# Kernel optimization log

Hardware: AMD Instinct MI355X
Metric: run time of the kernel (lower is better)

The kernel has to match this reference:

```python
import jax, jax.numpy as jnp
import numpy as np

B, T, BIN, D, S, L = 128, 512, 24, 256, 128, 2
MAX_LEN = 512.0   # config.max_length, used as attention score scale
EPS = 1e-6
P = 3.0           # GeM pooling power


def _sinusoid(t, dim, min_ts=1.0, max_ts=10000.0):
    # half sin / half cos geometric timescales (min_timescale..max_timescale)
    num = dim // 2
    inv = min_ts * jnp.exp(jnp.arange(num, dtype=jnp.float32) * (-np.log(max_ts / min_ts) / max(num - 1, 1)))
    ang = jnp.arange(t, dtype=jnp.float32)[:, None] * inv[None, :]        # [T, dim/2]
    return jnp.concatenate([jnp.sin(ang), jnp.cos(ang)], axis=-1)          # [T, dim]


def _rope(x):
    # rotate-half RoPE over last dim, positions along axis -2
    t, d = x.shape[-2], x.shape[-1]
    inv = 1.0 / (10000.0 ** (jnp.arange(0, d, 2, dtype=jnp.float32) / d))  # [d/2]
    ang = jnp.arange(t, dtype=jnp.float32)[:, None] * inv[None, :]         # [T, d/2]
    sin = jnp.concatenate([jnp.sin(ang), jnp.sin(ang)], axis=-1)
    cos = jnp.concatenate([jnp.cos(ang), jnp.cos(ang)], axis=-1)
    x1, x2 = jnp.split(x, 2, axis=-1)
    return x * cos + jnp.concatenate([-x2, x1], axis=-1) * sin


def setup_inputs() -> dict:
    key = jax.random.key(0)
    ks = jax.random.split(key, 12)
    std_in = 1.0 / np.sqrt(BIN)
    std_d = 1.0 / np.sqrt(D)
    return {
        "x": jax.random.uniform(ks[0], (B, T, BIN), dtype=jnp.float32),
        "pe_scale": jnp.ones((), jnp.float32),                                  # learnable PE scale
        "W_in": jax.random.normal(ks[1], (BIN, D), jnp.float32) * std_in,        # encoder_start
        "b_in": jnp.zeros((D,), jnp.float32),
        "norm_scale": jnp.ones((L,), jnp.float32),                               # ScaledNorm scalar per layer
        "W1": jax.random.normal(ks[2], (L, D, 2 * D + S), jnp.float32) * std_d,  # GAU in-proj
        "b1": jnp.zeros((L, 2 * D + S), jnp.float32),
        "gamma": jnp.ones((L, 2, S), jnp.float32),                               # q/k offset-scale
        "beta": jnp.zeros((L, 2, S), jnp.float32),
        "W2": jax.random.normal(ks[3], (L, D, D), jnp.float32) * std_d,          # GAU out-proj
        "b2": jnp.zeros((L, D), jnp.float32),
        "We": jax.random.normal(ks[4], (D, D), jnp.float32) * std_d,             # metric embedding
        "be": jnp.zeros((D,), jnp.float32),
    }


def reference(x, pe_scale, W_in, b_in, norm_scale, W1, b1, gamma, beta, W2, b2, We, be):
    # scaled sinusoidal positional embedding (additive)
    h = x + pe_scale * _sinusoid(x.shape[1], x.shape[2])
    # encoder start + swish
    h = jax.nn.swish(h @ W_in + b_in)                                   # [B,T,D]
    for i in range(L):  # GAU stack (attention-free gated attention units)
        shortcut = h
        hn = h * jax.lax.rsqrt(jnp.mean(h * h, axis=-1, keepdims=True) + EPS) * norm_scale[i]
        uv = jax.nn.swish(hn @ W1[i] + b1[i])                           # [B,T,2D+S]
        u, v, base = uv[..., :D], uv[..., D:2 * D], uv[..., 2 * D:]
        q = _rope(base * gamma[i, 0] + beta[i, 0])                      # [B,T,S]
        k = _rope(base * gamma[i, 1] + beta[i, 1])
        scores = jnp.einsum('bnd,bmd->bnm', q, k) / MAX_LEN             # [B,T,T]
        attn = jnp.square(jax.nn.relu(scores))                          # SqrReLU
        out = u * jnp.einsum('bnm,bme->bne', attn, v)                   # gated attention output
        h = shortcut + out @ W2[i] + b2[i]
    unpooled = h
    # generalized-mean pooling over sequence (p=3, clamp for stability)
    pooled = jnp.mean(jnp.clip(h, EPS, None) ** P, axis=1) ** (1.0 / P)  # [B,D]
    # metric embedding: linear + L2 normalize
    emb = pooled @ We + be
    emb = emb / jnp.linalg.norm(emb, axis=-1, keepdims=True)
    return emb, unpooled
```

## Files before the change

kernel.cpp:

```cpp
#include <hip/hip_runtime.h>
#include <hip/hip_bf16.h>

#define B_ 128
#define T_ 512
#define BIN_ 24
#define D_ 256
#define S_ 128
#define L_ 2
#define BT_ (B_*T_)

typedef __hip_bfloat16 bf16;
typedef __hip_bfloat162 bf162;
typedef __attribute__((ext_vector_type(8))) short bf16x8;
typedef __attribute__((ext_vector_type(4))) short s16x4;
typedef __attribute__((ext_vector_type(4))) float f32x4;

__device__ __forceinline__ float b2f(bf16 x){ return __bfloat162float(x); }
__device__ __forceinline__ bf16 f2b(float x){ return __float2bfloat16(x); }
__device__ __forceinline__ float swish(float v){
  float e = __builtin_amdgcn_exp2f(-1.442695040888963f * v);
  return v * __builtin_amdgcn_rcpf(1.f + e);
}
__device__ __forceinline__ void gld16(const bf16* g, bf16* l){
  __builtin_amdgcn_global_load_lds(
      (const __attribute__((address_space(1))) void*)g,
      (__attribute__((address_space(3))) void*)l, 16, 0, 0);
}

__global__ void tables_kernel(const float* pe_scale_ptr, float* pe_tab, float* rs, float* rc) {
  int t = blockIdx.x;
  int j = threadIdx.x;
  float ps = pe_scale_ptr[0];
  const float LOG1E4 = 9.210340371976184f;
  if (j < 64) {
    float inv = expf(-LOG1E4 * (float)j / 64.f);
    float ang = (float)t * inv;
    rs[t*64 + j] = sinf(ang);
    rc[t*64 + j] = cosf(ang);
  }
  if (j < BIN_) {
    int jj = (j < 12) ? j : (j - 12);
    float inv = expf(-LOG1E4 * (float)jj / 11.f);
    float ang = (float)t * inv;
    pe_tab[t*BIN_ + j] = ps * ((j < 12) ? sinf(ang) : cosf(ang));
  }
}

__global__ __launch_bounds__(256) void prep_kernel(const float* W1, const float* W2,
                                                   bf16* W1t, bf16* W2t) {
  int idx = blockIdx.x*256 + threadIdx.x;
  if (idx < 2*256*640) {
    int l = idx / (256*640); int rem = idx % (256*640);
    int k = rem / 640; int n = rem % 640;
    W1t[(size_t)l*640*256 + n*256 + k] = f2b(W1[idx]);
  }
  if (idx < 2*256*256) {
    int l = idx >> 16; int rem = idx & 65535;
    int k = rem >> 8; int n = rem & 255;
    W2t[(size_t)l*65536 + n*256 + k] = f2b(W2[idx]);
  }
}

__global__ __launch_bounds__(256) void init_kernel(float* rms1, float* pooled_raw) {
  int i = blockIdx.x*256 + threadIdx.x;
  if (i < BT_) rms1[i] = 0.f;
  if (i < B_*D_) pooled_raw[i] = 0.f;
}

__global__ __launch_bounds__(256) void embed_kernel(const float* x, const float* pe_tab,
                const float* W_in, const float* b_in, float* rms0, bf16* hb) {
  __shared__ float xr[8][BIN_];
  __shared__ float wsum[4][8];
  int tid = threadIdx.x;
  int row0 = blockIdx.x * 8;
  if (tid < 8*BIN_) {
    int r = tid / BIN_, k = tid % BIN_;
    int row = row0 + r;
    int t = row & (T_-1);
    xr[r][k] = x[(size_t)row*BIN_ + k] + pe_tab[t*BIN_ + k];
  }
  __syncthreads();
  int d = tid;
  float bi = b_in[d];
  float acc[8];
  #pragma unroll
  for (int r=0;r<8;r++) acc[r]=bi;
  #pragma unroll
  for (int k=0;k<BIN_;k++){
    float w = W_in[k*D_ + d];
    #pragma unroll
    for (int r=0;r<8;r++) acc[r] += xr[r][k]*w;
  }
  float sq[8];
  #pragma unroll
  for (int r=0;r<8;r++){
    float v = swish(acc[r]);
    hb[(size_t)(row0+r)*D_ + d] = f2b(v);
    sq[r] = v*v;
  }
  #pragma unroll
  for (int off=1; off<64; off<<=1)
    #pragma unroll
    for (int r=0;r<8;r++) sq[r] += __shfl_xor(sq[r], off);
  if ((tid&63)==0)
    #pragma unroll
    for (int r=0;r<8;r++) wsum[tid>>6][r] = sq[r];
  __syncthreads();
  if (tid < 8) rms0[row0+tid] = wsum[0][tid]+wsum[1][tid]+wsum[2][tid]+wsum[3][tid];
}

__global__ __launch_bounds__(256) void gemm1_mfma(const bf16* A, const bf16* Bt,
      const float* bias, const float* rmsraw, const float* norm_scale, int l,
      bf16* u, bf16* Vtg, bf16* basebuf) {
  __shared__ char smem[34816];
  bf16* As  = (bf16*)smem;
  bf16* Bs  = (bf16*)(smem + 16384);
  bf16* Ovl = (bf16*)smem;

  int tid = threadIdx.x;
  int w = tid>>6, lane = tid&63, r = lane&15, g = lane>>4;
  int wr = w>>1, wc = w&1;
  int dd = blockIdx.x; int xcd = dd&7, slot = dd>>3;
  int panel = xcd*64 + slot/5; int bx = slot%5;
  int row0 = panel*128, col0 = bx*128;

  int trl = 8*w + (lane>>3);
  int tcg = ((lane&7) ^ ((lane>>3)&7)) * 8;

  f32x4 acc[4][4];
  #pragma unroll
  for (int i=0;i<4;i++)
    #pragma unroll
    for (int j=0;j<4;j++) acc[i][j] = (f32x4){0.f,0.f,0.f,0.f};

  for (int k0=0; k0<D_; k0+=64) {
    #pragma unroll
    for (int i=0;i<4;i++){
      int tr = 32*i + trl;
      gld16(A  + (size_t)(row0+tr)*D_ + k0 + tcg, As + (32*i + 8*w)*64);
      gld16(Bt + (size_t)(col0+tr)*D_ + k0 + tcg, Bs + (32*i + 8*w)*64);
    }
    __syncthreads();
    #pragma unroll
    for (int kk=0; kk<2; kk++){
      bf16x8 a[4], b[4];
      #pragma unroll
      for (int i=0;i<4;i++){
        int ch = ((kk*4 + g) ^ (r&7)) * 8;
        a[i] = *(const bf16x8*)(As + (64*wr+16*i+r)*64 + ch);
        b[i] = *(const bf16x8*)(Bs + (64*wc+16*i+r)*64 + ch);
      }
      #pragma unroll
      for (int i=0;i<4;i++)
        #pragma unroll
        for (int j=0;j<4;j++)
          acc[i][j] = __builtin_amdgcn_mfma_f32_16x16x32_bf16(a[i], b[j], acc[i][j], 0,0,0);
    }
    __syncthreads();
  }

  float ns = norm_scale[l];
  #pragma unroll
  for (int i=0;i<4;i++){
    size_t grow0 = row0 + 64*wr + 16*i + 4*g;
    float4 rv = *(const float4*)(rmsraw + grow0);
    float sc[4];
    sc[0] = rsqrtf(rv.x*(1.f/D_) + 1e-6f) * ns;
    sc[1] = rsqrtf(rv.y*(1.f/D_) + 1e-6f) * ns;
    sc[2] = rsqrtf(rv.z*(1.f/D_) + 1e-6f) * ns;
    sc[3] = rsqrtf(rv.w*(1.f/D_) + 1e-6f) * ns;
    #pragma unroll
    for (int j=0;j<4;j++){
      int gcol = col0 + 64*wc + 16*j + r;
      float bv = bias[gcol];
      if (bx == 2 || bx == 3) {
        #pragma unroll
        for (int reg=0; reg<4; reg++){
          float v = swish(acc[i][j][reg]*sc[reg] + bv);
          Ovl[(64*wc+16*j+r)*136 + (64*wr+16*i+4*g+reg)] = f2b(v);
        }
      } else {
        #pragma unroll
        for (int reg=0; reg<4; reg++){
          float v = swish(acc[i][j][reg]*sc[reg] + bv);
          Ovl[(64*wr+16*i+4*g+reg)*136 + (64*wc+16*j+r)] = f2b(v);
        }
      }
    }
  }

  __syncthreads();
  if (bx == 2 || bx == 3) {
    size_t bb = row0 >> 9;
    int mg = row0 & 511;
    #pragma unroll
    for (int c=0;c<8;c++){
      int chunk = c*256 + tid;
      int e = chunk >> 4, mloc = (chunk & 15)*8;
      *(bf16x8*)(Vtg + bb*131072 + (size_t)(col0-256+e)*T_ + mg + mloc) =
        *(const bf16x8*)(Ovl + e*136 + mloc);
    }
  } else {
    #pragma unroll
    for (int c=0;c<8;c++){
      int chunk = c*256 + tid;
      int lr = chunk >> 4, lc = (chunk & 15)*8;
      bf16x8 v = *(const bf16x8*)(Ovl + lr*136 + lc);
      if (bx < 2)
        *(bf16x8*)(u + (size_t)(row0+lr)*D_ + col0 + lc) = v;
      else
        *(bf16x8*)(basebuf + (size_t)(row0+lr)*S_ + lc) = v;
    }
  }
}

__global__ __launch_bounds__(256) void qk_kernel(const bf16* basebuf, const float* gamma, const float* beta,
      int l, const float* rs, const float* rc, bf16* q, bf16* k) {
  int tid = threadIdx.x;
  int j = tid & 127;
  size_t row = (size_t)blockIdx.x*2 + (tid>>7);
  int t = (int)(row & (T_-1));
  int j2 = j ^ 64;
  float v0 = b2f(basebuf[row*S_ + j]);
  float v1 = b2f(basebuf[row*S_ + j2]);
  int jm = j & 63;
  float sn = rs[t*64 + jm], cs = rc[t*64 + jm];
  float sgn = (j < 64) ? -1.f : 1.f;
  const float* g  = gamma + l*2*S_;
  const float* bt = beta  + l*2*S_;
  float xq = v0*g[j]      + bt[j];
  float pq = v1*g[j2]     + bt[j2];
  q[row*S_ + j] = f2b(xq*cs + sgn*pq*sn);
  float xk = v0*g[S_+j]   + bt[S_+j];
  float pk = v1*g[S_+j2]  + bt[S_+j2];
  k[row*S_ + j] = f2b(xk*cs + sgn*pk*sn);
}

__global__ __launch_bounds__(512, 4) void attn_gemm2_fused(const bf16* q, const bf16* k,
      const bf16* Vtg, const bf16* u, const bf16* W2t, const float* bias,
      int mode, float* rms1, float* pooled_raw, float* outb, bf16* hb) {
  __shared__ char smem[67584];
  bf16* Ks = (bf16*)smem;
  bf16* Vt = (bf16*)(smem + 16384);
  bf16* Ps = (bf16*)(smem + 49152);
  bf16* Os = (bf16*)smem;

  int tid = threadIdx.x;
  int w = tid >> 6, l = tid & 63;
  int r = l & 15, g = l >> 4;
  int rgp = w & 3, eh = w >> 2;
  int xcd = blockIdx.x & 7, j0 = blockIdx.x >> 3;
  int b  = xcd*16 + (j0 >> 2);
  int nt = j0 & 3;
  size_t rowbase = (size_t)b * T_;
  int n0 = nt * 128;

  bf16x8 qf[4];
  const bf16* qrow = q + (rowbase + n0 + 16*w + r) * S_ + g*8;
  #pragma unroll
  for (int kk=0; kk<4; kk++) qf[kk] = *(const bf16x8*)(qrow + kk*32);

  f32x4 oacc[16];
  #pragma unroll
  for (int i=0;i<16;i++) oacc[i] = (f32x4){0.f,0.f,0.f,0.f};

  for (int m0 = 0; m0 < T_; m0 += 64) {
    #pragma unroll
    for (int i=0;i<2;i++){
      int chunk = i*512 + w*64 + l;
      int row = chunk >> 4, c = chunk & 15;
      gld16(k + (rowbase + m0 + row)*S_ + ((c ^ (row&7)) << 3),
            Ks + (i*512 + w*64)*8);
    }
    #pragma unroll
    for (int i=0;i<4;i++){
      int chunk = i*512 + w*64 + l;
      int e = chunk >> 3, c = chunk & 7;
      gld16(Vtg + (size_t)b*131072 + (size_t)e*T_ + m0 + ((c ^ (e&7)) << 3),
            Vt + (i*512 + w*64)*8);
    }
    __syncthreads();

    __builtin_amdgcn_s_setprio(1);
    #pragma unroll
    for (int nf=0; nf<4; nf++){
      f32x4 sacc = (f32x4){0.f,0.f,0.f,0.f};
      #pragma unroll
      for (int kk=0; kk<4; kk++){
        int ch = ((kk*4 + g) ^ (r&7)) * 8;
        bf16x8 kf = *(const bf16x8*)(Ks + (16*nf + r)*128 + ch);
        sacc = __builtin_amdgcn_mfma_f32_16x16x32_bf16(qf[kk], kf, sacc, 0,0,0);
      }
      #pragma unroll
      for (int reg=0; reg<4; reg++){
        float t = fmaxf(sacc[reg] * (1.f/512.f), 0.f);
        Ps[(16*w + 4*g + reg)*72 + 16*nf + r] = f2b(t*t);
      }
    }
    __builtin_amdgcn_s_setprio(0);
    __syncthreads();

    __builtin_amdgcn_s_setprio(1);
    #pragma unroll
    for (int ks=0; ks<2; ks++){
      bf16x8 pa0 = *(const bf16x8*)(Ps + (32*rgp      + r)*72 + ks*32 + g*8);
      bf16x8 pa1 = *(const bf16x8*)(Ps + (32*rgp + 16 + r)*72 + ks*32 + g*8);
      #pragma unroll
      for (int ef=0; ef<8; ef++){
        int e = 16*(8*eh + ef) + r;
        bf16x8 vb = *(const bf16x8*)(Vt + e*64 + (((4*ks + g) ^ (e&7)) << 3));
        oacc[ef]   = __builtin_amdgcn_mfma_f32_16x16x32_bf16(pa0, vb, oacc[ef],   0,0,0);
        oacc[8+ef] = __builtin_amdgcn_mfma_f32_16x16x32_bf16(pa1, vb, oacc[8+ef], 0,0,0);
      }
    }
    __builtin_amdgcn_s_setprio(0);
    __syncthreads();
  }

  size_t growbase = rowbase + n0;
  #pragma unroll
  for (int rr=0; rr<2; rr++)
    #pragma unroll
    for (int ef=0; ef<8; ef++)
      #pragma unroll
      for (int reg=0; reg<4; reg++)
        Os[(32*rgp + 16*rr + 4*g + reg)*264 + 16*(8*eh+ef) + r] = f2b(oacc[rr*8+ef][reg]);
  __syncthreads();
  #pragma unroll
  for (int i=0;i<8;i++){
    int chunk = i*512 + tid;
    int row = chunk >> 5, c = chunk & 31;
    bf16x8 uvv = *(const bf16x8*)(u + (growbase + row)*D_ + c*8);
    bf16x8 ov  = *(const bf16x8*)(Os + row*264 + c*8);
    bf16x8 res;
    #pragma unroll
    for (int e=0;e<8;e++)
      ((bf16*)&res)[e] = f2b(b2f(((bf16*)&ov)[e]) * b2f(((bf16*)&uvv)[e]));
    *(bf16x8*)(Os + row*264 + c*8) = res;
  }
  __syncthreads();

  f32x4 acc2[2][8];
  #pragma unroll
  for (int c2=0;c2<2;c2++)
    #pragma unroll
    for (int i=0;i<8;i++) acc2[c2][i] = (f32x4){0.f,0.f,0.f,0.f};
  __builtin_amdgcn_s_setprio(1);
  #pragma unroll
  for (int kc=0; kc<8; kc++){
    bf16x8 a0[8];
    #pragma unroll
    for (int i=0;i<8;i++)
      a0[i] = *(const bf16x8*)(Os + (16*i + r)*264 + kc*32 + g*8);
    #pragma unroll
    for (int chf=0; chf<2; chf++){
      bf16x8 wfr = *(const bf16x8*)(W2t + (size_t)(128*chf + 16*w + r)*256 + kc*32 + g*8);
      #pragma unroll
      for (int i=0;i<8;i++)
        acc2[chf][i] = __builtin_amdgcn_mfma_f32_16x16x32_bf16(a0[i], wfr, acc2[chf][i], 0,0,0);
    }
  }
  __builtin_amdgcn_s_setprio(0);

  #pragma unroll
  for (int chf=0; chf<2; chf++){
    int col = 128*chf + 16*w + r;
    float bv = bias[col];
    if (mode == 0) {
      #pragma unroll
      for (int i=0;i<8;i++){
        #pragma unroll
        for (int reg=0; reg<4; reg++){
          size_t row = growbase + 16*i + 4*g + reg;
          float hv = b2f(hb[row*D_ + col]) + acc2[chf][i][reg] + bv;
          hb[row*D_ + col] = f2b(hv);
          float ssum = hv*hv;
          ssum += __shfl_xor(ssum,1); ssum += __shfl_xor(ssum,2);
          ssum += __shfl_xor(ssum,4); ssum += __shfl_xor(ssum,8);
          if (r == 0) atomicAdd(rms1 + row, ssum);
        }
      }
    } else {
      float psum = 0.f;
      #pragma unroll
      for (int i=0;i<8;i++){
        #pragma unroll
        for (int reg=0; reg<4; reg++){
          size_t row = growbase + 16*i + 4*g + reg;
          float hv = b2f(hb[row*D_ + col]) + acc2[chf][i][reg] + bv;
          outb[row*D_ + col] = hv;
          float cv = fmaxf(hv, 1e-6f);
          psum += cv*cv*cv;
        }
      }
      psum += __shfl_xor(psum,16); psum += __shfl_xor(psum,32);
      if (g == 0) atomicAdd(pooled_raw + b*D_ + col, psum);
    }
  }
}

__global__ __launch_bounds__(256) void emb_kernel(const float* pooled_raw, const float* We,
      const float* be, float* out) {
  __shared__ float pr[D_];
  __shared__ float red[256];
  int b = blockIdx.x, j = threadIdx.x;
  pr[j] = cbrtf(pooled_raw[b*D_+j] * (1.f/T_));
  __syncthreads();
  float acc = be[j];
  for (int kk=0;kk<D_;kk++) acc += pr[kk]*We[kk*D_+j];
  red[j] = acc*acc;
  __syncthreads();
  for (int off=128; off>0; off>>=1){
    if (j<off) red[j]+=red[j+off];
    __syncthreads();
  }
  out[b*D_+j] = acc * rsqrtf(red[0]);
}

extern "C" void kernel_launch(void* const* d_in, const int* in_sizes, int n_in,
                              void* d_out, int out_size, void* d_ws, size_t ws_size,
                              hipStream_t stream) {
  const float* x         = (const float*)d_in[0];
  const float* pe_scale  = (const float*)d_in[1];
  const float* W_in      = (const float*)d_in[2];
  const float* b_in      = (const float*)d_in[3];
  const float* norm_scale= (const float*)d_in[4];
  const float* W1        = (const float*)d_in[5];
  const float* b1        = (const float*)d_in[6];
  const float* gamma     = (const float*)d_in[7];
  const float* beta      = (const float*)d_in[8];
  const float* W2        = (const float*)d_in[9];
  const float* b2        = (const float*)d_in[10];
  const float* We        = (const float*)d_in[11];
  const float* be        = (const float*)d_in[12];

  char* ws = (char*)d_ws;
  bf16*  hb      = (bf16*)(ws);
  bf16*  u       = (bf16*)(ws + 33554432);
  bf16*  Vtg     = (bf16*)(ws + 67108864);
  bf16*  basebuf = (bf16*)(ws + 100663296);
  bf16*  q       = (bf16*)(ws + 117440512);
  bf16*  kbuf    = (bf16*)(ws + 134217728);
  float* pe_tab  = (float*)(ws + 150994944);
  float* rs_tab  = (float*)(ws + 151044096);
  float* rc_tab  = (float*)(ws + 151175168);
  float* pooled_raw = (float*)(ws + 151306240);
  float* rms0    = (float*)(ws + 151437312);
  float* rms1    = (float*)(ws + 151699456);
  bf16*  W1t     = (bf16*)(ws + 151961600);
  bf16*  W2t     = (bf16*)(ws + 152616960);

  tables_kernel<<<T_, 64, 0, stream>>>(pe_scale, pe_tab, rs_tab, rc_tab);
  prep_kernel<<<1280, 256, 0, stream>>>(W1, W2, W1t, W2t);
  init_kernel<<<BT_/256, 256, 0, stream>>>(rms1, pooled_raw);
  embed_kernel<<<BT_/8, 256, 0, stream>>>(x, pe_tab, W_in, b_in, rms0, hb);
  float* outb = (float*)d_out + B_*D_;
  for (int l=0; l<L_; l++) {
    gemm1_mfma<<<BT_/128*5, 256, 0, stream>>>(hb, W1t + (size_t)l*640*D_, b1 + l*640,
        l ? rms1 : rms0, norm_scale, l, u, Vtg, basebuf);
    qk_kernel<<<BT_/2, 256, 0, stream>>>(basebuf, gamma, beta, l, rs_tab, rc_tab, q, kbuf);
    attn_gemm2_fused<<<B_*4, 512, 0, stream>>>(q, kbuf, Vtg, u,
        W2t + (size_t)l*D_*D_, b2 + l*D_, l, rms1, pooled_raw, outb, hb);
  }
  emb_kernel<<<B_, 256, 0, stream>>>(pooled_raw, We, be, (float*)d_out);
}
```

Before: 331.6 us.

## Halve attention query tile and key chunk to double block count

Reduces the fused attention+out-proj kernel's per-block query tile from 128 to 64 rows and the key/value chunk from 64 to 32, launching twice as many blocks with half the shared memory and fewer accumulators. The warp-to-work mapping, the LDS swizzles for V and the P staging stride are reworked to match. The aim is more blocks resident per CU and better latency hiding. In exchange each K/V tile is reloaded by twice as many blocks, each chunk does less MFMA work per barrier, and W2 fragments are re-read per smaller row tile.

```diff
diff --git a/kernel.cpp b/kernel.cpp
--- a/kernel.cpp
+++ b/kernel.cpp
@@ -236,81 +236,77 @@
   k[row*S_ + j] = f2b(xk*cs + sgn*pk*sn);
 }
 
-__global__ __launch_bounds__(512, 4) void attn_gemm2_fused(const bf16* q, const bf16* k,
+__global__ __launch_bounds__(512, 6) void attn_gemm2_fused(const bf16* q, const bf16* k,
       const bf16* Vtg, const bf16* u, const bf16* W2t, const float* bias,
       int mode, float* rms1, float* pooled_raw, float* outb, bf16* hb) {
-  __shared__ char smem[67584];
+  __shared__ char smem[33792];
   bf16* Ks = (bf16*)smem;
-  bf16* Vt = (bf16*)(smem + 16384);
-  bf16* Ps = (bf16*)(smem + 49152);
+  bf16* Vt = (bf16*)(smem + 8192);
+  bf16* Ps = (bf16*)(smem + 24576);
   bf16* Os = (bf16*)smem;
 
   int tid = threadIdx.x;
   int w = tid >> 6, l = tid & 63;
   int r = l & 15, g = l >> 4;
-  int rgp = w & 3, eh = w >> 2;
+  int wq = w & 3, nfh = w >> 2;
+  int rgp2 = w & 1, eh2 = w >> 1;
   int xcd = blockIdx.x & 7, j0 = blockIdx.x >> 3;
-  int b  = xcd*16 + (j0 >> 2);
-  int nt = j0 & 3;
+  int b  = xcd*16 + (j0 >> 3);
+  int nt = j0 & 7;
   size_t rowbase = (size_t)b * T_;
-  int n0 = nt * 128;
+  int n0 = nt * 64;
 
   bf16x8 qf[4];
-  const bf16* qrow = q + (rowbase + n0 + 16*w + r) * S_ + g*8;
+  const bf16* qrow = q + (rowbase + n0 + 16*wq + r) * S_ + g*8;
   #pragma unroll
   for (int kk=0; kk<4; kk++) qf[kk] = *(const bf16x8*)(qrow + kk*32);
 
-  f32x4 oacc[16];
-  #pragma unroll
-  for (int i=0;i<16;i++) oacc[i] = (f32x4){0.f,0.f,0.f,0.f};
-
-  for (int m0 = 0; m0 < T_; m0 += 64) {
+  f32x4 oacc[8];
+  #pragma unroll
+  for (int i=0;i<8;i++) oacc[i] = (f32x4){0.f,0.f,0.f,0.f};
+
+  for (int m0 = 0; m0 < T_; m0 += 32) {
+    {
+      int row = tid >> 4, c = tid & 15;
+      gld16(k + (rowbase + m0 + row)*S_ + ((c ^ (row&7)) << 3), Ks + w*512);
+    }
     #pragma unroll
     for (int i=0;i<2;i++){
-      int chunk = i*512 + w*64 + l;
-      int row = chunk >> 4, c = chunk & 15;
-      gld16(k + (rowbase + m0 + row)*S_ + ((c ^ (row&7)) << 3),
-            Ks + (i*512 + w*64)*8);
-    }
-    #pragma unroll
-    for (int i=0;i<4;i++){
-      int chunk = i*512 + w*64 + l;
-      int e = chunk >> 3, c = chunk & 7;
-      gld16(Vtg + (size_t)b*131072 + (size_t)e*T_ + m0 + ((c ^ (e&7)) << 3),
+      int chunk = i*512 + tid;
+      int e = chunk >> 2, c = chunk & 3;
+      gld16(Vtg + (size_t)b*131072 + (size_t)e*T_ + m0 + ((c ^ (e&3)) << 3),
             Vt + (i*512 + w*64)*8);
     }
     __syncthreads();
 
     __builtin_amdgcn_s_setprio(1);
-    #pragma unroll
-    for (int nf=0; nf<4; nf++){
+    {
       f32x4 sacc = (f32x4){0.f,0.f,0.f,0.f};
       #pragma unroll
       for (int kk=0; kk<4; kk++){
         int ch = ((kk*4 + g) ^ (r&7)) * 8;
-        bf16x8 kf = *(const bf16x8*)(Ks + (16*nf + r)*128 + ch);
+        bf16x8 kf = *(const bf16x8*)(Ks + (16*nfh + r)*128 + ch);
         sacc = __builtin_amdgcn_mfma_f32_16x16x32_bf16(qf[kk], kf, sacc, 0,0,0);
       }
       #pragma unroll
       for (int reg=0; reg<4; reg++){
         float t = fmaxf(sacc[reg] * (1.f/512.f), 0.f);
-        Ps[(16*w + 4*g + reg)*72 + 16*nf + r] = f2b(t*t);
+        Ps[(16*wq + 4*g + reg)*40 + 16*nfh + r] = f2b(t*t);
       }
     }
     __builtin_amdgcn_s_setprio(0);
     __syncthreads();
 
     __builtin_amdgcn_s_setprio(1);
-    #pragma unroll
-    for (int ks=0; ks<2; ks++){
-      bf16x8 pa0 = *(const bf16x8*)(Ps + (32*rgp      + r)*72 + ks*32 + g*8);
-      bf16x8 pa1 = *(const bf16x8*)(Ps + (32*rgp + 16 + r)*72 + ks*32 + g*8);
-      #pragma unroll
-      for (int ef=0; ef<8; ef++){
-        int e = 16*(8*eh + ef) + r;
-        bf16x8 vb = *(const bf16x8*)(Vt + e*64 + (((4*ks + g) ^ (e&7)) << 3));
+    {
+      bf16x8 pa0 = *(const bf16x8*)(Ps + (32*rgp2      + r)*40 + g*8);
+      bf16x8 pa1 = *(const bf16x8*)(Ps + (32*rgp2 + 16 + r)*40 + g*8);
+      #pragma unroll
+      for (int ef=0; ef<4; ef++){
+        int e = 16*(4*eh2 + ef) + r;
+        bf16x8 vb = *(const bf16x8*)(Vt + e*32 + ((g ^ (e&3)) << 3));
         oacc[ef]   = __builtin_amdgcn_mfma_f32_16x16x32_bf16(pa0, vb, oacc[ef],   0,0,0);
-        oacc[8+ef] = __builtin_amdgcn_mfma_f32_16x16x32_bf16(pa1, vb, oacc[8+ef], 0,0,0);
+        oacc[4+ef] = __builtin_amdgcn_mfma_f32_16x16x32_bf16(pa1, vb, oacc[4+ef], 0,0,0);
       }
     }
     __builtin_amdgcn_s_setprio(0);
@@ -321,13 +317,13 @@
   #pragma unroll
   for (int rr=0; rr<2; rr++)
     #pragma unroll
-    for (int ef=0; ef<8; ef++)
+    for (int ef=0; ef<4; ef++)
       #pragma unroll
       for (int reg=0; reg<4; reg++)
-        Os[(32*rgp + 16*rr + 4*g + reg)*264 + 16*(8*eh+ef) + r] = f2b(oacc[rr*8+ef][reg]);
-  __syncthreads();
-  #pragma unroll
-  for (int i=0;i<8;i++){
+        Os[(32*rgp2 + 16*rr + 4*g + reg)*264 + 16*(4*eh2+ef) + r] = f2b(oacc[rr*4+ef][reg]);
+  __syncthreads();
+  #pragma unroll
+  for (int i=0;i<4;i++){
     int chunk = i*512 + tid;
     int row = chunk >> 5, c = chunk & 31;
     bf16x8 uvv = *(const bf16x8*)(u + (growbase + row)*D_ + c*8);
@@ -340,23 +336,23 @@
   }
   __syncthreads();
 
-  f32x4 acc2[2][8];
+  f32x4 acc2[2][4];
   #pragma unroll
   for (int c2=0;c2<2;c2++)
     #pragma unroll
-    for (int i=0;i<8;i++) acc2[c2][i] = (f32x4){0.f,0.f,0.f,0.f};
+    for (int i=0;i<4;i++) acc2[c2][i] = (f32x4){0.f,0.f,0.f,0.f};
   __builtin_amdgcn_s_setprio(1);
   #pragma unroll
   for (int kc=0; kc<8; kc++){
-    bf16x8 a0[8];
-    #pragma unroll
-    for (int i=0;i<8;i++)
+    bf16x8 a0[4];
+    #pragma unroll
+    for (int i=0;i<4;i++)
       a0[i] = *(const bf16x8*)(Os + (16*i + r)*264 + kc*32 + g*8);
     #pragma unroll
     for (int chf=0; chf<2; chf++){
       bf16x8 wfr = *(const bf16x8*)(W2t + (size_t)(128*chf + 16*w + r)*256 + kc*32 + g*8);
       #pragma unroll
-      for (int i=0;i<8;i++)
+      for (int i=0;i<4;i++)
         acc2[chf][i] = __builtin_amdgcn_mfma_f32_16x16x32_bf16(a0[i], wfr, acc2[chf][i], 0,0,0);
     }
   }
@@ -368,7 +364,7 @@
     float bv = bias[col];
     if (mode == 0) {
       #pragma unroll
-      for (int i=0;i<8;i++){
+      for (int i=0;i<4;i++){
         #pragma unroll
         for (int reg=0; reg<4; reg++){
           size_t row = growbase + 16*i + 4*g + reg;
@@ -383,7 +379,7 @@
     } else {
       float psum = 0.f;
       #pragma unroll
-      for (int i=0;i<8;i++){
+      for (int i=0;i<4;i++){
         #pragma unroll
         for (int reg=0; reg<4; reg++){
           size_t row = growbase + 16*i + 4*g + reg;
@@ -459,7 +455,7 @@
     gemm1_mfma<<<BT_/128*5, 256, 0, stream>>>(hb, W1t + (size_t)l*640*D_, b1 + l*640,
         l ? rms1 : rms0, norm_scale, l, u, Vtg, basebuf);
     qk_kernel<<<BT_/2, 256, 0, stream>>>(basebuf, gamma, beta, l, rs_tab, rc_tab, q, kbuf);
-    attn_gemm2_fused<<<B_*4, 512, 0, stream>>>(q, kbuf, Vtg, u,
+    attn_gemm2_fused<<<B_*8, 512, 0, stream>>>(q, kbuf, Vtg, u,
         W2t + (size_t)l*D_*D_, b2 + l*D_, l, rms1, pooled_raw, outb, hb);
   }
   emb_kernel<<<B_, 256, 0, stream>>>(pooled_raw, We, be, (float*)d_out);
```

Measured after the change: 378.5 us. 14.1% more time.
